# Optimization experiments

Hardware: AMD Instinct MI355X
Metric: run time of the kernel (lower is better)

Reference implementation:

```python
import jax, jax.numpy as jnp
import numpy as np

B, S, D_IN, D_OUT, DEPTH = 4, 2048, 2048, 2048, 11
N_NODES = 2 ** (DEPTH + 1) - 1  # 4095


def setup_inputs() -> dict:
    key = jax.random.key(0)
    k1, k2, k3 = jax.random.split(key, 3)
    x = jax.random.normal(k1, (B, S, D_IN), dtype=jnp.float32)
    # scale weights like Linear init (~1/sqrt(fan_in)) to keep logits sane
    w_in = jax.random.normal(k2, (N_NODES, D_IN), dtype=jnp.float32) * (1.0 / np.sqrt(D_IN))
    w_out = jax.random.normal(k3, (D_OUT, N_NODES), dtype=jnp.float32) * (1.0 / np.sqrt(N_NODES))
    return {"x": x, "w_in": w_in, "w_out": w_out}


def reference(x, w_in, w_out):
    # x: [B,S,D_in]; w_in: [n_nodes, D_in]; w_out: [D_out, n_nodes]
    b, s, _ = x.shape
    cur = jnp.zeros((b, s), dtype=jnp.int32)
    nodes, logits = [], []
    for _ in range(DEPTH + 1):  # fixed, small depth loop (12 iters)
        nodes.append(cur)
        coeffs = w_in[cur]                       # [B,S,D_in] data-dependent gather
        score = jnp.einsum('bsd,bsd->bs', x, coeffs)  # per-token dot product
        logits.append(score)
        cur = cur * 2 + (score >= 0).astype(jnp.int32) + 1
    all_nodes = jnp.stack(nodes, axis=-1)        # [B,S,depth+1]
    all_logits = jnp.stack(logits, axis=-1)      # [B,S,depth+1]
    sel = w_out.T[all_nodes]                     # [B,S,depth+1,D_out]
    mlp1 = jax.nn.gelu(all_logits, approximate=False)  # torch nn.GELU default = exact erf
    return jnp.einsum('bsl,bslw->bsw', mlp1, sel)      # [B,S,D_out]
```

## Files before the change

kernel.cpp:

```cpp
#include <hip/hip_runtime.h>


#define D_IN    2048
#define D_OUT   2048
#define DEPTHP1 12
#define N_NODES 4095
#define N_TOK   8192
#define N_LEAF  2048

__global__ __launch_bounds__(256) void transpose_wout64(
    const float* __restrict__ in, float* __restrict__ out) {
    __shared__ float tile[64][65];
    const int n0 = blockIdx.x * 64;
    const int j0 = blockIdx.y * 64;
    const int tx = threadIdx.x;
    const int ty = threadIdx.y;
    const int n = n0 + tx;
#pragma unroll
    for (int k = 0; k < 16; k++) {
        const int r = ty * 16 + k;
        if (n < N_NODES) tile[r][tx] = in[(size_t)(j0 + r) * N_NODES + n];
    }
    __syncthreads();
#pragma unroll
    for (int k = 0; k < 16; k++) {
        const int r = ty * 16 + k;
        const int nn = n0 + r;
        if (nn < N_NODES) out[(size_t)nn * D_OUT + (j0 + tx)] = tile[tx][r];
    }
}

__device__ __forceinline__ float dot8(const float4 (&w)[8],
                                      const float4* __restrict__ xw,
                                      int lane) {
    float p0 = 0.f, p1 = 0.f, p2 = 0.f, p3 = 0.f;
#pragma unroll
    for (int c = 0; c < 8; c++) {
        const float4 wc = w[c];
        const float4 xc = xw[lane + 64 * c];
        float* p = (c < 2) ? &p0 : (c < 4) ? &p1 : (c < 6) ? &p2 : &p3;
        *p += wc.x * xc.x + wc.y * xc.y + wc.z * xc.z + wc.w * xc.w;
    }
    return (p0 + p1) + (p2 + p3);
}

__global__ __launch_bounds__(256, 3) void phaseA(
    const float* __restrict__ x,
    const float* __restrict__ w_in,
    float* __restrict__ g_all,
    int* __restrict__ leaf,
    int* __restrict__ hist) {
    extern __shared__ float xs[];
    const int wave  = threadIdx.x >> 6;
    const int lane  = threadIdx.x & 63;
    const int token = blockIdx.x * 4 + wave;

    float4* xw = (float4*)(xs) + wave * (D_IN / 4);
    const float4* xrow = (const float4*)(x + (size_t)token * D_IN);
#pragma unroll
    for (int c = 0; c < 8; c++) xw[lane + 64 * c] = xrow[lane + 64 * c];

    const float4* w4 = (const float4*)w_in;
    float4 a0[8], b0[8], a1[8], b1[8];

#pragma unroll
    for (int c = 0; c < 8; c++) a0[c] = w4[lane + 64 * c];
#pragma unroll
    for (int c = 0; c < 8; c++) a1[c] = w4[512 * 1 + lane + 64 * c];
#pragma unroll
    for (int c = 0; c < 8; c++) b1[c] = w4[512 * 2 + lane + 64 * c];

    int cur, dir;
    {
        float part = dot8(a0, xw, lane);
#pragma unroll
        for (int off = 32; off >= 1; off >>= 1) part += __shfl_xor(part, off, 64);
        const float score = part;
        dir = (score >= 0.f) ? 1 : 0;
        cur = 1 + dir;
        const float g = 0.5f * score * (1.0f + erff(score * 0.70710678118654752f));
        if (lane == 0) g_all[token * DEPTHP1 + 0] = g;
    }

#pragma unroll
    for (int l = 1; l < DEPTHP1; l++) {
        if (l < DEPTHP1 - 1) {
            const int c0 = 2 * cur + 1;
            if (l & 1) {
#pragma unroll
                for (int c = 0; c < 8; c++)
                    a0[c] = w4[(size_t)c0 * 512 + lane + 64 * c];
#pragma unroll
                for (int c = 0; c < 8; c++)
                    b0[c] = w4[(size_t)(c0 + 1) * 512 + lane + 64 * c];
            } else {
#pragma unroll
                for (int c = 0; c < 8; c++)
                    a1[c] = w4[(size_t)c0 * 512 + lane + 64 * c];
#pragma unroll
                for (int c = 0; c < 8; c++)
                    b1[c] = w4[(size_t)(c0 + 1) * 512 + lane + 64 * c];
            }
        }
        float part;
        if (l & 1) part = dir ? dot8(b1, xw, lane) : dot8(a1, xw, lane);
        else       part = dir ? dot8(b0, xw, lane) : dot8(a0, xw, lane);
#pragma unroll
        for (int off = 32; off >= 1; off >>= 1) part += __shfl_xor(part, off, 64);
        const float score = part;
        dir = (score >= 0.f) ? 1 : 0;
        cur = 2 * cur + 1 + dir;
        const float g = 0.5f * score * (1.0f + erff(score * 0.70710678118654752f));
        if (lane == 0) g_all[token * DEPTHP1 + l] = g;
    }
    if (lane == 0) {
        const int leafid = ((cur - 1) >> 1) - (N_LEAF - 1);
        leaf[token] = leafid;
        atomicAdd(&hist[leafid], 1);
    }
}

__global__ __launch_bounds__(256) void init_counts(int* __restrict__ p) {
    const int i = blockIdx.x * 256 + threadIdx.x;
    if (i < 2 * N_LEAF) p[i] = 0;
}

__global__ __launch_bounds__(256) void scan2048(
    const int* __restrict__ hist, int* __restrict__ offsets ) {
    __shared__ int vals[N_LEAF];
    __shared__ int partial[256];
    const int t = threadIdx.x;
    int sum = 0;
#pragma unroll
    for (int k = 0; k < 8; k++) {
        const int v = hist[t * 8 + k];
        vals[t * 8 + k] = v;
        sum += v;
    }
    partial[t] = sum;
    __syncthreads();
    for (int off = 1; off < 256; off <<= 1) {
        const int v  = partial[t];
        const int vo = (t >= off) ? partial[t - off] : 0;
        __syncthreads();
        partial[t] = v + vo;
        __syncthreads();
    }
    int base = (t > 0) ? partial[t - 1] : 0;
#pragma unroll
    for (int k = 0; k < 8; k++) {
        offsets[t * 8 + k] = base;
        base += vals[t * 8 + k];
    }
    if (t == 255) offsets[N_LEAF] = base;
}

__global__ __launch_bounds__(256) void scatter_tokens(
    const int* __restrict__ leaf, const int* __restrict__ offsets,
    int* __restrict__ cnt, const float* __restrict__ g_all,
    int* __restrict__ order, float* __restrict__ g_sorted) {
    const int t = blockIdx.x * 256 + threadIdx.x;
    if (t < N_TOK) {
        const int lf = leaf[t];
        const int pos = offsets[lf] + atomicAdd(&cnt[lf], 1);
        order[pos] = t;
#pragma unroll
        for (int l = 0; l < DEPTHP1; l++)
            g_sorted[(size_t)pos * DEPTHP1 + l] = g_all[(size_t)t * DEPTHP1 + l];
    }
}

__global__ __launch_bounds__(256, 2) void phaseB(
    const float* __restrict__ w_out_t,
    const float* __restrict__ g_sorted,
    const int* __restrict__ order,
    const int* __restrict__ offsets,
    float* __restrict__ out) {
    const int lf = ((blockIdx.x & 7) << 8) | (blockIdx.x >> 3);
    const int start = offsets[lf];
    const int end   = offsets[lf + 1];
    if (start == end) return;
    const int t = threadIdx.x;

    int nodes[DEPTHP1];
    const int L = lf + N_LEAF;
#pragma unroll
    for (int l = 0; l < DEPTHP1; l++) nodes[l] = (L >> (DEPTHP1 - 1 - l)) - 1;

    for (int cs = start; cs < end; cs += 8) {
        const int T = end - cs;
        float acc[8][8];
#pragma unroll
        for (int tt = 0; tt < 8; tt++)
#pragma unroll
            for (int k = 0; k < 8; k++) acc[tt][k] = 0.f;

#pragma unroll
        for (int l = 0; l < DEPTHP1; l++) {
            const float4* wr = (const float4*)(w_out_t + (size_t)nodes[l] * D_OUT);
            const float4 w0 = wr[t * 2 + 0];
            const float4 w1 = wr[t * 2 + 1];
#pragma unroll
            for (int tt = 0; tt < 8; tt++) {
                const float g = (tt < T)
                    ? g_sorted[(size_t)(cs + tt) * DEPTHP1 + l] : 0.f;
                acc[tt][0] += g * w0.x; acc[tt][1] += g * w0.y;
                acc[tt][2] += g * w0.z; acc[tt][3] += g * w0.w;
                acc[tt][4] += g * w1.x; acc[tt][5] += g * w1.y;
                acc[tt][6] += g * w1.z; acc[tt][7] += g * w1.w;
            }
        }
#pragma unroll
        for (int tt = 0; tt < 8; tt++) {
            if (tt < T) {
                const int tok = order[cs + tt];
                float4* po = (float4*)(out + (size_t)tok * D_OUT + t * 8);
                float4 o0, o1;
                o0.x = acc[tt][0]; o0.y = acc[tt][1];
                o0.z = acc[tt][2]; o0.w = acc[tt][3];
                o1.x = acc[tt][4]; o1.y = acc[tt][5];
                o1.z = acc[tt][6]; o1.w = acc[tt][7];
                po[0] = o0; po[1] = o1;
            }
        }
    }
}

template <bool TRANSPOSED>
__global__ __launch_bounds__(256) void fff_fused(
    const float* __restrict__ x, const float* __restrict__ w_in,
    const float* __restrict__ w_out, float* __restrict__ out) {
    const int wave  = threadIdx.x >> 6;
    const int lane  = threadIdx.x & 63;
    const int token = blockIdx.x * 4 + wave;
    const float4* xrow = (const float4*)(x + (size_t)token * D_IN);
    float xf[32];
#pragma unroll
    for (int c = 0; c < 8; c++) {
        float4 xc = xrow[lane + 64 * c];
        xf[c * 4 + 0] = xc.x; xf[c * 4 + 1] = xc.y;
        xf[c * 4 + 2] = xc.z; xf[c * 4 + 3] = xc.w;
    }
    float acc[32];
#pragma unroll
    for (int k = 0; k < 32; k++) acc[k] = 0.f;
    int cur = 0;
#pragma unroll
    for (int l = 0; l < DEPTHP1; l++) {
        const float4* wrow = (const float4*)(w_in + (size_t)cur * D_IN);
        float part = 0.f;
#pragma unroll
        for (int c = 0; c < 8; c++) {
            float4 wc = wrow[lane + 64 * c];
            part += wc.x * xf[c * 4 + 0]; part += wc.y * xf[c * 4 + 1];
            part += wc.z * xf[c * 4 + 2]; part += wc.w * xf[c * 4 + 3];
        }
#pragma unroll
        for (int off = 32; off >= 1; off >>= 1) part += __shfl_xor(part, off, 64);
        const float score = part;
        const float g = 0.5f * score * (1.0f + erff(score * 0.70710678118654752f));
        if (TRANSPOSED) {
            const float4* orow = (const float4*)(w_out + (size_t)cur * D_OUT);
#pragma unroll
            for (int c = 0; c < 8; c++) {
                float4 oc = orow[lane + 64 * c];
                acc[c * 4 + 0] += g * oc.x; acc[c * 4 + 1] += g * oc.y;
                acc[c * 4 + 2] += g * oc.z; acc[c * 4 + 3] += g * oc.w;
            }
        } else {
#pragma unroll
            for (int c = 0; c < 8; c++)
#pragma unroll
                for (int k = 0; k < 4; k++) {
                    const int j = (lane + 64 * c) * 4 + k;
                    acc[c * 4 + k] += g * w_out[(size_t)j * N_NODES + cur];
                }
        }
        cur = 2 * cur + 1 + (score >= 0.f ? 1 : 0);
    }
    float4* outrow = (float4*)(out + (size_t)token * D_OUT);
#pragma unroll
    for (int c = 0; c < 8; c++) {
        float4 o;
        o.x = acc[c * 4 + 0]; o.y = acc[c * 4 + 1];
        o.z = acc[c * 4 + 2]; o.w = acc[c * 4 + 3];
        outrow[lane + 64 * c] = o;
    }
}

extern "C" void kernel_launch(void* const* d_in, const int* in_sizes, int n_in,
                              void* d_out, int out_size, void* d_ws, size_t ws_size,
                              hipStream_t stream) {
    (void)in_sizes; (void)n_in; (void)out_size;
    const float* x     = (const float*)d_in[0];
    const float* w_in  = (const float*)d_in[1];
    const float* w_out = (const float*)d_in[2];
    float* out = (float*)d_out;

    const size_t wt_bytes   = (size_t)N_NODES * D_OUT * sizeof(float);
    const size_t g_bytes    = (size_t)N_TOK * DEPTHP1 * sizeof(float);
    const size_t leaf_bytes = (size_t)N_TOK * sizeof(int);
    const size_t ord_bytes  = (size_t)N_TOK * sizeof(int);
    const size_t hist_bytes = (size_t)N_LEAF * sizeof(int);
    const size_t cnt_bytes  = (size_t)N_LEAF * sizeof(int);
    const size_t offs_bytes = (size_t)(N_LEAF + 1) * sizeof(int);
    const size_t gs_bytes   = g_bytes;
    const size_t need = wt_bytes + g_bytes + leaf_bytes + ord_bytes +
                        hist_bytes + cnt_bytes + offs_bytes + gs_bytes + 64;

    if (ws_size >= need) {
        char* p = (char*)d_ws;
        float* w_out_t  = (float*)p;  p += wt_bytes;
        float* g_all    = (float*)p;  p += g_bytes;
        int*   leaf     = (int*)p;    p += leaf_bytes;
        int*   order    = (int*)p;    p += ord_bytes;
        int*   hist     = (int*)p;    p += hist_bytes;
        int*   cnt      = (int*)p;    p += cnt_bytes;
        int*   offsets  = (int*)p;    p += offs_bytes;
        float* g_sorted = (float*)p;

        init_counts<<<(2 * N_LEAF + 255) / 256, 256, 0, stream>>>(hist);
        transpose_wout64<<<dim3((N_NODES + 63) / 64, D_OUT / 64), dim3(64, 4),
                           0, stream>>>(w_out, w_out_t);
        phaseA<<<N_TOK / 4, 256, 4 * D_IN * sizeof(float), stream>>>(
            x, w_in, g_all, leaf, hist);
        scan2048<<<1, 256, 0, stream>>>(hist, offsets);
        scatter_tokens<<<N_TOK / 256, 256, 0, stream>>>(leaf, offsets, cnt,
                                                        g_all, order, g_sorted);
        phaseB<<<N_LEAF, 256, 0, stream>>>(w_out_t, g_sorted, order, offsets, out);
    } else if (ws_size >= wt_bytes) {
        float* w_out_t = (float*)d_ws;
        transpose_wout64<<<dim3((N_NODES + 63) / 64, D_OUT / 64), dim3(64, 4),
                           0, stream>>>(w_out, w_out_t);
        fff_fused<true><<<N_TOK / 4, 256, 0, stream>>>(x, w_in, w_out_t, out);
    } else {
        fff_fused<false><<<N_TOK / 4, 256, 0, stream>>>(x, w_in, w_out, out);
    }
}
```

Before: 265.6 us.

## Fuse w_out transpose into tree-traversal kernel and use DPP wave reduction

Merges the w_out transpose and the phase-A tree traversal into one launch, with odd blocks doing transpose tiles and even blocks doing token traversal, so the transpose overlaps the latency-bound gather work and one launch is dropped. The per-level wave reduction is replaced with DPP row operations plus a lane-63 broadcast instead of six xor shuffles. The double-buffered a0/b0/a1/b1 register sets are collapsed into two buffers with a per-element select, cutting register pressure at the cost of select instructions. Transpose blocks now request the same 32KB dynamic shared memory, which may limit occupancy.

```diff
diff --git a/kernel.cpp b/kernel.cpp
--- a/kernel.cpp
+++ b/kernel.cpp
@@ -8,108 +8,124 @@
 #define N_TOK   8192
 #define N_LEAF  2048
 
-__global__ __launch_bounds__(256) void transpose_wout64(
-    const float* __restrict__ in, float* __restrict__ out) {
-    __shared__ float tile[64][65];
-    const int n0 = blockIdx.x * 64;
-    const int j0 = blockIdx.y * 64;
-    const int tx = threadIdx.x;
-    const int ty = threadIdx.y;
-    const int n = n0 + tx;
-#pragma unroll
-    for (int k = 0; k < 16; k++) {
-        const int r = ty * 16 + k;
-        if (n < N_NODES) tile[r][tx] = in[(size_t)(j0 + r) * N_NODES + n];
-    }
-    __syncthreads();
-#pragma unroll
-    for (int k = 0; k < 16; k++) {
-        const int r = ty * 16 + k;
-        const int nn = n0 + r;
-        if (nn < N_NODES) out[(size_t)nn * D_OUT + (j0 + tx)] = tile[tx][r];
-    }
-}
-
-__device__ __forceinline__ float dot8(const float4 (&w)[8],
-                                      const float4* __restrict__ xw,
-                                      int lane) {
-    float p0 = 0.f, p1 = 0.f, p2 = 0.f, p3 = 0.f;
-#pragma unroll
-    for (int c = 0; c < 8; c++) {
-        const float4 wc = w[c];
-        const float4 xc = xw[lane + 64 * c];
-        float* p = (c < 2) ? &p0 : (c < 4) ? &p1 : (c < 6) ? &p2 : &p3;
-        *p += wc.x * xc.x + wc.y * xc.y + wc.z * xc.z + wc.w * xc.w;
-    }
-    return (p0 + p1) + (p2 + p3);
-}
-
-__global__ __launch_bounds__(256, 3) void phaseA(
+template <int CTRL, int RMASK, int BMASK>
+__device__ __forceinline__ float dpp_add(float x) {
+    union U { float f; int i; };
+    U s; s.f = x;
+    U d; d.i = __builtin_amdgcn_update_dpp(0, s.i, CTRL, RMASK, BMASK, false);
+    return x + d.f;
+}
+__device__ __forceinline__ float wave_sum_bcast(float part) {
+    part = dpp_add<0x111, 0xf, 0xf>(part);
+    part = dpp_add<0x112, 0xf, 0xf>(part);
+    part = dpp_add<0x114, 0xf, 0xe>(part);
+    part = dpp_add<0x118, 0xf, 0xc>(part);
+    part = dpp_add<0x142, 0xa, 0xf>(part);
+    part = dpp_add<0x143, 0xc, 0xf>(part);
+    return __shfl(part, 63, 64);
+}
+
+__global__ __launch_bounds__(256, 3) void fatA(
     const float* __restrict__ x,
     const float* __restrict__ w_in,
+    const float* __restrict__ w_out,
+    float* __restrict__ w_out_t,
     float* __restrict__ g_all,
     int* __restrict__ leaf,
     int* __restrict__ hist) {
-    extern __shared__ float xs[];
+    extern __shared__ float smem[];
+
+    if (blockIdx.x & 1) {
+        float (*tile)[65] = (float(*)[65])smem;
+        const int tid = blockIdx.x >> 1;
+        const int n0 = (tid & 63) * 64;
+        const int j0 = (tid >> 6) * 64;
+        const int tx = threadIdx.x & 63;
+        const int ty = threadIdx.x >> 6;
+        const int n = n0 + tx;
+#pragma unroll
+        for (int k = 0; k < 16; k++) {
+            const int r = ty * 16 + k;
+            if (n < N_NODES) tile[r][tx] = w_out[(size_t)(j0 + r) * N_NODES + n];
+        }
+        __syncthreads();
+#pragma unroll
+        for (int k = 0; k < 16; k++) {
+            const int r = ty * 16 + k;
+            const int nn = n0 + r;
+            if (nn < N_NODES) w_out_t[(size_t)nn * D_OUT + (j0 + tx)] = tile[tx][r];
+        }
+        return;
+    }
+
     const int wave  = threadIdx.x >> 6;
     const int lane  = threadIdx.x & 63;
-    const int token = blockIdx.x * 4 + wave;
-
-    float4* xw = (float4*)(xs) + wave * (D_IN / 4);
+    const int token = (blockIdx.x >> 1) * 4 + wave;
+
+    float4* xw = (float4*)smem + wave * (D_IN / 4);
     const float4* xrow = (const float4*)(x + (size_t)token * D_IN);
 #pragma unroll
     for (int c = 0; c < 8; c++) xw[lane + 64 * c] = xrow[lane + 64 * c];
 
     const float4* w4 = (const float4*)w_in;
-    float4 a0[8], b0[8], a1[8], b1[8];
-
-#pragma unroll
-    for (int c = 0; c < 8; c++) a0[c] = w4[lane + 64 * c];
-#pragma unroll
-    for (int c = 0; c < 8; c++) a1[c] = w4[512 * 1 + lane + 64 * c];
-#pragma unroll
-    for (int c = 0; c < 8; c++) b1[c] = w4[512 * 2 + lane + 64 * c];
-
-    int cur, dir;
+    float4 wa[8], wb[8];
+
+    float4 r0[8];
+#pragma unroll
+    for (int c = 0; c < 8; c++) r0[c] = w4[lane + 64 * c];
+#pragma unroll
+    for (int c = 0; c < 8; c++) wa[c] = w4[512 * 1 + lane + 64 * c];
+#pragma unroll
+    for (int c = 0; c < 8; c++) wb[c] = w4[512 * 2 + lane + 64 * c];
+
+    int cur;
+    bool takeB;
     {
-        float part = dot8(a0, xw, lane);
-#pragma unroll
-        for (int off = 32; off >= 1; off >>= 1) part += __shfl_xor(part, off, 64);
-        const float score = part;
-        dir = (score >= 0.f) ? 1 : 0;
-        cur = 1 + dir;
+        float p0 = 0.f, p1 = 0.f, p2 = 0.f, p3 = 0.f;
+#pragma unroll
+        for (int c = 0; c < 8; c++) {
+            const float4 wc = r0[c];
+            const float4 xc = xw[lane + 64 * c];
+            float* p = (c < 2) ? &p0 : (c < 4) ? &p1 : (c < 6) ? &p2 : &p3;
+            *p += wc.x * xc.x + wc.y * xc.y + wc.z * xc.z + wc.w * xc.w;
+        }
+        const float score = wave_sum_bcast((p0 + p1) + (p2 + p3));
+        takeB = (score >= 0.f);
+        cur = takeB ? 2 : 1;
         const float g = 0.5f * score * (1.0f + erff(score * 0.70710678118654752f));
         if (lane == 0) g_all[token * DEPTHP1 + 0] = g;
     }
 
 #pragma unroll
     for (int l = 1; l < DEPTHP1; l++) {
+        float4 sel[8];
+#pragma unroll
+        for (int c = 0; c < 8; c++) {
+            sel[c].x = takeB ? wb[c].x : wa[c].x;
+            sel[c].y = takeB ? wb[c].y : wa[c].y;
+            sel[c].z = takeB ? wb[c].z : wa[c].z;
+            sel[c].w = takeB ? wb[c].w : wa[c].w;
+        }
         if (l < DEPTHP1 - 1) {
             const int c0 = 2 * cur + 1;
-            if (l & 1) {
-#pragma unroll
-                for (int c = 0; c < 8; c++)
-                    a0[c] = w4[(size_t)c0 * 512 + lane + 64 * c];
-#pragma unroll
-                for (int c = 0; c < 8; c++)
-                    b0[c] = w4[(size_t)(c0 + 1) * 512 + lane + 64 * c];
-            } else {
-#pragma unroll
-                for (int c = 0; c < 8; c++)
-                    a1[c] = w4[(size_t)c0 * 512 + lane + 64 * c];
-#pragma unroll
-                for (int c = 0; c < 8; c++)
-                    b1[c] = w4[(size_t)(c0 + 1) * 512 + lane + 64 * c];
-            }
-        }
-        float part;
-        if (l & 1) part = dir ? dot8(b1, xw, lane) : dot8(a1, xw, lane);
-        else       part = dir ? dot8(b0, xw, lane) : dot8(a0, xw, lane);
-#pragma unroll
-        for (int off = 32; off >= 1; off >>= 1) part += __shfl_xor(part, off, 64);
-        const float score = part;
-        dir = (score >= 0.f) ? 1 : 0;
-        cur = 2 * cur + 1 + dir;
+#pragma unroll
+            for (int c = 0; c < 8; c++)
+                wa[c] = w4[(size_t)c0 * 512 + lane + 64 * c];
+#pragma unroll
+            for (int c = 0; c < 8; c++)
+                wb[c] = w4[(size_t)(c0 + 1) * 512 + lane + 64 * c];
+        }
+        float p0 = 0.f, p1 = 0.f, p2 = 0.f, p3 = 0.f;
+#pragma unroll
+        for (int c = 0; c < 8; c++) {
+            const float4 wc = sel[c];
+            const float4 xc = xw[lane + 64 * c];
+            float* p = (c < 2) ? &p0 : (c < 4) ? &p1 : (c < 6) ? &p2 : &p3;
+            *p += wc.x * xc.x + wc.y * xc.y + wc.z * xc.z + wc.w * xc.w;
+        }
+        const float score = wave_sum_bcast((p0 + p1) + (p2 + p3));
+        takeB = (score >= 0.f);
+        cur = 2 * cur + 1 + (takeB ? 1 : 0);
         const float g = 0.5f * score * (1.0f + erff(score * 0.70710678118654752f));
         if (lane == 0) g_all[token * DEPTHP1 + l] = g;
     }
@@ -226,6 +242,28 @@
     }
 }
 
+__global__ __launch_bounds__(256) void transpose_wout64(
+    const float* __restrict__ in, float* __restrict__ out) {
+    __shared__ float tile[64][65];
+    const int n0 = blockIdx.x * 64;
+    const int j0 = blockIdx.y * 64;
+    const int tx = threadIdx.x & 63;
+    const int ty = threadIdx.x >> 6;
+    const int n = n0 + tx;
+#pragma unroll
+    for (int k = 0; k < 16; k++) {
+        const int r = ty * 16 + k;
+        if (n < N_NODES) tile[r][tx] = in[(size_t)(j0 + r) * N_NODES + n];
+    }
+    __syncthreads();
+#pragma unroll
+    for (int k = 0; k < 16; k++) {
+        const int r = ty * 16 + k;
+        const int nn = n0 + r;
+        if (nn < N_NODES) out[(size_t)nn * D_OUT + (j0 + tx)] = tile[tx][r];
+    }
+}
+
 template <bool TRANSPOSED>
 __global__ __launch_bounds__(256) void fff_fused(
     const float* __restrict__ x, const float* __restrict__ w_in,
@@ -320,17 +358,15 @@
         float* g_sorted = (float*)p;
 
         init_counts<<<(2 * N_LEAF + 255) / 256, 256, 0, stream>>>(hist);
-        transpose_wout64<<<dim3((N_NODES + 63) / 64, D_OUT / 64), dim3(64, 4),
-                           0, stream>>>(w_out, w_out_t);
-        phaseA<<<N_TOK / 4, 256, 4 * D_IN * sizeof(float), stream>>>(
-            x, w_in, g_all, leaf, hist);
+        fatA<<<4096, 256, 32768, stream>>>(x, w_in, w_out, w_out_t,
+                                           g_all, leaf, hist);
         scan2048<<<1, 256, 0, stream>>>(hist, offsets);
         scatter_tokens<<<N_TOK / 256, 256, 0, stream>>>(leaf, offsets, cnt,
                                                         g_all, order, g_sorted);
         phaseB<<<N_LEAF, 256, 0, stream>>>(w_out_t, g_sorted, order, offsets, out);
     } else if (ws_size >= wt_bytes) {
         float* w_out_t = (float*)d_ws;
-        transpose_wout64<<<dim3((N_NODES + 63) / 64, D_OUT / 64), dim3(64, 4),
+        transpose_wout64<<<dim3((N_NODES + 63) / 64, D_OUT / 64), 256,
                            0, stream>>>(w_out, w_out_t);
         fff_fused<true><<<N_TOK / 4, 256, 0, stream>>>(x, w_in, w_out_t, out);
     } else {
```

Measured after the change: 312.8 us. 1.18x slower.
